# Optimization experiments

Hardware: AMD Instinct MI355X
Metric: run time of the kernel (lower is better)

Reference implementation:

```python
import jax, jax.numpy as jnp
import numpy as np


def setup_inputs() -> dict:
    key = jax.random.key(0)
    k1, k2 = jax.random.split(key)
    B, N, M = 16, 4096, 4096
    points1 = jax.random.normal(k1, (B, N, 3), dtype=jnp.float32)
    points2 = jax.random.normal(k2, (B, M, 3), dtype=jnp.float32)
    return {"points1": points1, "points2": points2}


def reference(points1, points2):
    # Mathematically equal to sum((x - y)^2) without materializing (B,N,M,3).
    w1 = 1.0
    w2 = 1.0
    sq1 = jnp.sum(points1 * points1, axis=-1)  # (B, N)
    sq2 = jnp.sum(points2 * points2, axis=-1)  # (B, M)
    cross = jnp.einsum("bnd,bmd->bnm", points1, points2)  # (B, N, M)
    dist = sq1[:, :, None] + sq2[:, None, :] - 2.0 * cross  # (B, N, M)
    dist_min1 = jnp.min(dist, axis=2)  # nearest in points2 for each point1
    dist_min2 = jnp.min(dist, axis=1)  # nearest in points1 for each point2
    B = points1.shape[0]
    return (w1 * jnp.sum(dist_min1) + w2 * jnp.sum(dist_min2)) / B
```

## Files before the change

### kernel.cpp

```cpp
#include <hip/hip_runtime.h>

typedef _Float16 half8 __attribute__((ext_vector_type(8)));
typedef float f32x16 __attribute__((ext_vector_type(16)));

#define NPTS   4096
#define BATCH  16
#define BLOCK  256
#define CHUNK  2048
#define NCHUNK 2
#define NBLK   512

__global__ __launch_bounds__(BLOCK, 2) void chamfer_mfma_kernel(
    const float* __restrict__ p1, const float* __restrict__ p2,
    float* __restrict__ partial)
{
    __shared__ half8 REC[CHUNK];

    const int tid  = threadIdx.x;
    const int lane = tid & 63;
    const int n    = lane & 31;
    const int grp  = lane >> 5;
    const int wv   = tid >> 6;
    const int blk  = blockIdx.x;
    const int j    = blk & 15;
    const int b    = (blk >> 4) & 15;
    const int dir  = blk >> 8;

    const float* selfp  = (dir == 0 ? p1 : p2) + (size_t)b * NPTS * 3;
    const float* otherp = (dir == 0 ? p2 : p1) + (size_t)b * NPTS * 3;

    const int base = j * 256 + wv * 64;
    half8 a0, a1;
    float ssq01;
    {
        const int i0 = (base + n) * 3, i1 = (base + 32 + n) * 3;
        float x0 = selfp[i0], y0 = selfp[i0 + 1], z0 = selfp[i0 + 2];
        float x1 = selfp[i1], y1 = selfp[i1 + 1], z1 = selfp[i1 + 2];
        ssq01 = fmaf(x0, x0, fmaf(y0, y0, z0 * z0)) +
                fmaf(x1, x1, fmaf(y1, y1, z1 * z1));
        _Float16 hx0 = (_Float16)x0, hy0 = (_Float16)y0, hz0 = (_Float16)z0;
        _Float16 lx0 = (_Float16)(x0 - (float)hx0);
        _Float16 ly0 = (_Float16)(y0 - (float)hy0);
        _Float16 lz0 = (_Float16)(z0 - (float)hz0);
        _Float16 hx1 = (_Float16)x1, hy1 = (_Float16)y1, hz1 = (_Float16)z1;
        _Float16 lx1 = (_Float16)(x1 - (float)hx1);
        _Float16 ly1 = (_Float16)(y1 - (float)hy1);
        _Float16 lz1 = (_Float16)(z1 - (float)hz1);
        const _Float16 c0 = (_Float16)0.f, c1 = (_Float16)1.f;
        if (grp == 0) {
            a0[0]=hx0; a0[1]=hy0; a0[2]=hz0; a0[3]=c0; a0[4]=c0; a0[5]=c0; a0[6]=c1; a0[7]=c0;
            a1[0]=hx1; a1[1]=hy1; a1[2]=hz1; a1[3]=c0; a1[4]=c0; a1[5]=c0; a1[6]=c1; a1[7]=c0;
        } else {
            a0[0]=lx0; a0[1]=ly0; a0[2]=lz0; a0[3]=hx0; a0[4]=hy0; a0[5]=hz0; a0[6]=c0; a0[7]=c1;
            a1[0]=lx1; a1[1]=ly1; a1[2]=lz1; a1[3]=hx1; a1[4]=hy1; a1[5]=hz1; a1[6]=c0; a1[7]=c1;
        }
    }

    f32x16 m0, m1, zc;
#pragma unroll
    for (int r = 0; r < 16; ++r) { m0[r] = 3.4e38f; m1[r] = 3.4e38f; zc[r] = 0.f; }

    for (int c = 0; c < NCHUNK; ++c) {
        __syncthreads();
        {
            const float4* src = (const float4*)(otherp + (size_t)c * CHUNK * 3);
            float4 v0 = src[tid * 6 + 0], v1 = src[tid * 6 + 1];
            float4 v2 = src[tid * 6 + 2], v3 = src[tid * 6 + 3];
            float4 v4 = src[tid * 6 + 4], v5 = src[tid * 6 + 5];
            float ox[8] = {v0.x, v0.w, v1.z, v2.y, v3.x, v3.w, v4.z, v5.y};
            float oy[8] = {v0.y, v1.x, v1.w, v2.z, v3.y, v4.x, v4.w, v5.z};
            float oz[8] = {v0.z, v1.y, v2.x, v2.w, v3.z, v4.y, v5.x, v5.w};
#pragma unroll
            for (int k = 0; k < 8; ++k) {
                float gx = -2.f * ox[k], gy = -2.f * oy[k], gz = -2.f * oz[k];
                float q  = fmaf(ox[k], ox[k], fmaf(oy[k], oy[k], oz[k] * oz[k]));
                _Float16 ghx = (_Float16)gx, ghy = (_Float16)gy, ghz = (_Float16)gz;
                half8 r;
                r[0] = ghx; r[1] = ghy; r[2] = ghz;
                r[3] = (_Float16)(gx - (float)ghx);
                r[4] = (_Float16)(gy - (float)ghy);
                r[5] = (_Float16)(gz - (float)ghz);
                _Float16 qh = (_Float16)q;
                r[6] = qh;
                r[7] = (_Float16)(q - (float)qh);
                REC[tid * 8 + k] = r;
            }
        }
        __syncthreads();
        const half8* rp = REC + n;
#pragma unroll 2
        for (int g = 0; g < 32; ++g) {
            half8 b0 = rp[g * 64];
            half8 b1 = rp[g * 64 + 32];
            f32x16 o00 = __builtin_amdgcn_mfma_f32_32x32x16_f16(a0, b0, zc, 0, 0, 0);
            f32x16 o01 = __builtin_amdgcn_mfma_f32_32x32x16_f16(a0, b1, zc, 0, 0, 0);
            f32x16 o10 = __builtin_amdgcn_mfma_f32_32x32x16_f16(a1, b0, zc, 0, 0, 0);
            f32x16 o11 = __builtin_amdgcn_mfma_f32_32x32x16_f16(a1, b1, zc, 0, 0, 0);
#pragma unroll
            for (int r = 0; r < 16; ++r) {
                m0[r] = fminf(fminf(o00[r], o01[r]), m0[r]);
                m1[r] = fminf(fminf(o10[r], o11[r]), m1[r]);
            }
        }
    }

#pragma unroll
    for (int mask = 1; mask <= 16; mask <<= 1) {
#pragma unroll
        for (int r = 0; r < 16; ++r) {
            m0[r] = fminf(m0[r], __shfl_xor((float)m0[r], mask, 64));
            m1[r] = fminf(m1[r], __shfl_xor((float)m1[r], mask, 64));
        }
    }
    float rowsum = 0.f;
#pragma unroll
    for (int r = 0; r < 16; ++r) rowsum += m0[r] + m1[r];
    rowsum += __shfl_xor(rowsum, 32, 64);

    float sv = grp ? 0.f : ssq01;
#pragma unroll
    for (int mask = 1; mask <= 16; mask <<= 1) sv += __shfl_xor(sv, mask, 64);

    if (lane == 0) partial[blk * 4 + wv] = rowsum + sv;
}

__global__ __launch_bounds__(256) void chamfer_reduce(
    const float* __restrict__ partial, float* __restrict__ out)
{
    float s = 0.f;
    for (int i = threadIdx.x; i < NBLK * 4; i += 256) s += partial[i];
#pragma unroll
    for (int off = 32; off > 0; off >>= 1) s += __shfl_down(s, off, 64);
    __shared__ float ws4[4];
    int lane = threadIdx.x & 63, wv = threadIdx.x >> 6;
    if (lane == 0) ws4[wv] = s;
    __syncthreads();
    if (threadIdx.x == 0)
        out[0] = (ws4[0] + ws4[1] + ws4[2] + ws4[3]) * (1.0f / BATCH);
}

extern "C" void kernel_launch(void* const* d_in, const int* in_sizes, int n_in,
                              void* d_out, int out_size, void* d_ws, size_t ws_size,
                              hipStream_t stream) {
    const float* p1 = (const float*)d_in[0];
    const float* p2 = (const float*)d_in[1];
    float* out = (float*)d_out;
    float* partial = (float*)d_ws;

    chamfer_mfma_kernel<<<dim3(NBLK), dim3(BLOCK), 0, stream>>>(p1, p2, partial);
    chamfer_reduce<<<dim3(1), dim3(256), 0, stream>>>(partial, out);
}
```

Measured before the change: 77.97 us.

## Compute distance tile once for both directions with column atomicMin reductions

Instead of computing the full distance matrix twice (once per direction), each block computes a tile of p1 rows against all p2 points once. It takes row minima in registers and column minima through shuffle plus LDS atomicMin on order-preserving integer keys, then merges them into a global per-batch column-key array. A prep kernel precomputes fp16 hi/lo encodings of p2 into workspace, and the main kernel streams them into LDS with double-buffered global_load_lds. This halves the MFMA work, but adds column reduction ALU, LDS/global atomics, an extra launch and a larger final reduction.

```diff
diff --git a/kernel.cpp b/kernel.cpp
--- a/kernel.cpp
+++ b/kernel.cpp
@@ -1,142 +1,205 @@
 #include <hip/hip_runtime.h>
+#include <stdint.h>
 
 typedef _Float16 half8 __attribute__((ext_vector_type(8)));
 typedef float f32x16 __attribute__((ext_vector_type(16)));
 
 #define NPTS   4096
 #define BATCH  16
-#define BLOCK  256
-#define CHUNK  2048
-#define NCHUNK 2
-#define NBLK   512
-
-__global__ __launch_bounds__(BLOCK, 2) void chamfer_mfma_kernel(
-    const float* __restrict__ p1, const float* __restrict__ p2,
-    float* __restrict__ partial)
+#define TILES  32
+#define BLOCK  512
+#define NBLK   (BATCH * TILES)
+#define CHUNK  1024
+#define NCHUNK (NPTS / CHUNK)
+
+#define REC0_OFF    0
+#define REC1_OFF    (BATCH * NPTS * 16)
+#define COLKEY_OFF  (2 * BATCH * NPTS * 16)
+#define ROWPART_OFF (COLKEY_OFF + BATCH * NPTS * 4)
+
+__device__ __forceinline__ void gll16(const void* g, void* l) {
+    __builtin_amdgcn_global_load_lds(
+        (const __attribute__((address_space(1))) uint32_t*)g,
+        (__attribute__((address_space(3))) uint32_t*)l, 16, 0, 0);
+}
+
+__device__ __forceinline__ uint32_t fkey(float f) {
+    uint32_t u = __float_as_uint(f);
+    return u ^ ((uint32_t)((int32_t)u >> 31) | 0x80000000u);
+}
+__device__ __forceinline__ float funkey(uint32_t k) {
+    uint32_t u = (k & 0x80000000u) ? (k ^ 0x80000000u) : ~k;
+    return __uint_as_float(u);
+}
+
+__device__ __forceinline__ float rmin16(f32x16 o) {
+    float a = fminf(fminf(o[0],  o[1]),  fminf(o[2],  o[3]));
+    float b = fminf(fminf(o[4],  o[5]),  fminf(o[6],  o[7]));
+    float c = fminf(fminf(o[8],  o[9]),  fminf(o[10], o[11]));
+    float d = fminf(fminf(o[12], o[13]), fminf(o[14], o[15]));
+    return fminf(fminf(a, b), fminf(c, d));
+}
+
+__global__ __launch_bounds__(256) void chamfer_prep(
+    const float* __restrict__ p2, uint8_t* __restrict__ ws)
 {
-    __shared__ half8 REC[CHUNK];
+    const int idx = blockIdx.x * 256 + threadIdx.x;
+    const float x = p2[idx * 3], y = p2[idx * 3 + 1], z = p2[idx * 3 + 2];
+    const float gx = -2.f * x, gy = -2.f * y, gz = -2.f * z;
+    const float q  = fmaf(x, x, fmaf(y, y, z * z));
+    _Float16 ghx = (_Float16)gx, ghy = (_Float16)gy, ghz = (_Float16)gz;
+    _Float16 glx = (_Float16)(gx - (float)ghx);
+    _Float16 gly = (_Float16)(gy - (float)ghy);
+    _Float16 glz = (_Float16)(gz - (float)ghz);
+    _Float16 qh = (_Float16)q, ql = (_Float16)(q - (float)qh);
+    const _Float16 one = (_Float16)1.f;
+    half8 r0, r1;
+    r0[0]=ghx; r0[1]=ghy; r0[2]=ghz; r0[3]=one; r0[4]=one; r0[5]=glx; r0[6]=gly; r0[7]=glz;
+    r1[0]=ghx; r1[1]=ghy; r1[2]=ghz; r1[3]=glx; r1[4]=gly; r1[5]=glz; r1[6]=qh;  r1[7]=ql;
+    ((half8*)(ws + REC0_OFF))[idx] = r0;
+    ((half8*)(ws + REC1_OFF))[idx] = r1;
+    ((uint32_t*)(ws + COLKEY_OFF))[idx] = 0xFFFFFFFFu;
+}
+
+__global__ __launch_bounds__(BLOCK, 4) void chamfer_main(
+    const float* __restrict__ p1, uint8_t* __restrict__ ws)
+{
+    __shared__ half8    R0b[2][CHUNK];
+    __shared__ half8    R1b[2][CHUNK];
+    __shared__ uint32_t colKeyL[NPTS];
 
     const int tid  = threadIdx.x;
     const int lane = tid & 63;
     const int n    = lane & 31;
     const int grp  = lane >> 5;
     const int wv   = tid >> 6;
+    const int sg   = wv >> 1;
+    const int gh   = wv & 1;
     const int blk  = blockIdx.x;
-    const int j    = blk & 15;
-    const int b    = (blk >> 4) & 15;
-    const int dir  = blk >> 8;
-
-    const float* selfp  = (dir == 0 ? p1 : p2) + (size_t)b * NPTS * 3;
-    const float* otherp = (dir == 0 ? p2 : p1) + (size_t)b * NPTS * 3;
-
-    const int base = j * 256 + wv * 64;
-    half8 a0, a1;
-    float ssq01;
+    const int tile = blk & (TILES - 1);
+    const int b    = blk >> 5;
+
+    const float* selfp = p1 + (size_t)b * NPTS * 3;
+
+    half8 a;
     {
-        const int i0 = (base + n) * 3, i1 = (base + 32 + n) * 3;
-        float x0 = selfp[i0], y0 = selfp[i0 + 1], z0 = selfp[i0 + 2];
-        float x1 = selfp[i1], y1 = selfp[i1 + 1], z1 = selfp[i1 + 2];
-        ssq01 = fmaf(x0, x0, fmaf(y0, y0, z0 * z0)) +
-                fmaf(x1, x1, fmaf(y1, y1, z1 * z1));
-        _Float16 hx0 = (_Float16)x0, hy0 = (_Float16)y0, hz0 = (_Float16)z0;
-        _Float16 lx0 = (_Float16)(x0 - (float)hx0);
-        _Float16 ly0 = (_Float16)(y0 - (float)hy0);
-        _Float16 lz0 = (_Float16)(z0 - (float)hz0);
-        _Float16 hx1 = (_Float16)x1, hy1 = (_Float16)y1, hz1 = (_Float16)z1;
-        _Float16 lx1 = (_Float16)(x1 - (float)hx1);
-        _Float16 ly1 = (_Float16)(y1 - (float)hy1);
-        _Float16 lz1 = (_Float16)(z1 - (float)hz1);
-        const _Float16 c0 = (_Float16)0.f, c1 = (_Float16)1.f;
-        if (grp == 0) {
-            a0[0]=hx0; a0[1]=hy0; a0[2]=hz0; a0[3]=c0; a0[4]=c0; a0[5]=c0; a0[6]=c1; a0[7]=c0;
-            a1[0]=hx1; a1[1]=hy1; a1[2]=hz1; a1[3]=c0; a1[4]=c0; a1[5]=c0; a1[6]=c1; a1[7]=c0;
-        } else {
-            a0[0]=lx0; a0[1]=ly0; a0[2]=lz0; a0[3]=hx0; a0[4]=hy0; a0[5]=hz0; a0[6]=c0; a0[7]=c1;
-            a1[0]=lx1; a1[1]=ly1; a1[2]=lz1; a1[3]=hx1; a1[4]=hy1; a1[5]=hz1; a1[6]=c0; a1[7]=c1;
+        const int s = tile * 128 + sg * 32 + n;
+        const float x = selfp[s*3], y = selfp[s*3+1], z = selfp[s*3+2];
+        const float ss = fmaf(x, x, fmaf(y, y, z * z));
+        _Float16 hx = (_Float16)x, hy = (_Float16)y, hz = (_Float16)z;
+        _Float16 lx = (_Float16)(x - (float)hx);
+        _Float16 ly = (_Float16)(y - (float)hy);
+        _Float16 lz = (_Float16)(z - (float)hz);
+        _Float16 sh = (_Float16)ss, sl = (_Float16)(ss - (float)sh);
+        const _Float16 one = (_Float16)1.f;
+        if (grp == 0) { a[0]=hx; a[1]=hy; a[2]=hz; a[3]=sh; a[4]=sl; a[5]=lx; a[6]=ly; a[7]=lz; }
+        else          { a[0]=lx; a[1]=ly; a[2]=lz; a[3]=hx; a[4]=hy; a[5]=hz; a[6]=one; a[7]=one; }
+    }
+
+    for (int i = tid; i < NPTS; i += BLOCK) colKeyL[i] = 0xFFFFFFFFu;
+
+    f32x16 m0, zc;
+#pragma unroll
+    for (int r = 0; r < 16; ++r) { m0[r] = 3.4e38f; zc[r] = 0.f; }
+
+    const uint8_t* gsrcBase = ws + (wv < 4 ? REC0_OFF : REC1_OFF)
+                            + (size_t)b * NPTS * 16 + (size_t)(wv & 3) * 4096
+                            + (size_t)lane * 16;
+    {
+        char* l = (char*)(wv < 4 ? &R0b[0][0] : &R1b[0][0]) + (wv & 3) * 4096;
+        const uint8_t* g = gsrcBase;
+        gll16(g, l); gll16(g + 1024, l + 1024);
+        gll16(g + 2048, l + 2048); gll16(g + 3072, l + 3072);
+    }
+    __syncthreads();
+
+    for (int c = 0; c < NCHUNK; ++c) {
+        const int cb = c & 1;
+        if (c + 1 < NCHUNK) {
+            char* l = (char*)(wv < 4 ? &R0b[cb ^ 1][0] : &R1b[cb ^ 1][0]) + (wv & 3) * 4096;
+            const uint8_t* g = gsrcBase + (size_t)(c + 1) * 16384;
+            gll16(g, l); gll16(g + 1024, l + 1024);
+            gll16(g + 2048, l + 2048); gll16(g + 3072, l + 3072);
         }
-    }
-
-    f32x16 m0, m1, zc;
-#pragma unroll
-    for (int r = 0; r < 16; ++r) { m0[r] = 3.4e38f; m1[r] = 3.4e38f; zc[r] = 0.f; }
-
-    for (int c = 0; c < NCHUNK; ++c) {
-        __syncthreads();
-        {
-            const float4* src = (const float4*)(otherp + (size_t)c * CHUNK * 3);
-            float4 v0 = src[tid * 6 + 0], v1 = src[tid * 6 + 1];
-            float4 v2 = src[tid * 6 + 2], v3 = src[tid * 6 + 3];
-            float4 v4 = src[tid * 6 + 4], v5 = src[tid * 6 + 5];
-            float ox[8] = {v0.x, v0.w, v1.z, v2.y, v3.x, v3.w, v4.z, v5.y};
-            float oy[8] = {v0.y, v1.x, v1.w, v2.z, v3.y, v4.x, v4.w, v5.z};
-            float oz[8] = {v0.z, v1.y, v2.x, v2.w, v3.z, v4.y, v5.x, v5.w};
-#pragma unroll
-            for (int k = 0; k < 8; ++k) {
-                float gx = -2.f * ox[k], gy = -2.f * oy[k], gz = -2.f * oz[k];
-                float q  = fmaf(ox[k], ox[k], fmaf(oy[k], oy[k], oz[k] * oz[k]));
-                _Float16 ghx = (_Float16)gx, ghy = (_Float16)gy, ghz = (_Float16)gz;
-                half8 r;
-                r[0] = ghx; r[1] = ghy; r[2] = ghz;
-                r[3] = (_Float16)(gx - (float)ghx);
-                r[4] = (_Float16)(gy - (float)ghy);
-                r[5] = (_Float16)(gz - (float)ghz);
-                _Float16 qh = (_Float16)q;
-                r[6] = qh;
-                r[7] = (_Float16)(q - (float)qh);
-                REC[tid * 8 + k] = r;
-            }
+        const half8* rp = (grp ? &R1b[cb][0] : &R0b[cb][0]) + gh * 512 + n;
+        const int abase = c * CHUNK + gh * 512 + grp * 32 + n;
+#pragma unroll 2
+        for (int k = 0; k < 8; ++k) {
+            half8 b0 = rp[k * 64];
+            half8 b1 = rp[k * 64 + 32];
+            f32x16 o0 = __builtin_amdgcn_mfma_f32_32x32x16_f16(a, b0, zc, 0, 0, 0);
+            f32x16 o1 = __builtin_amdgcn_mfma_f32_32x32x16_f16(a, b1, zc, 0, 0, 0);
+#pragma unroll
+            for (int r = 0; r < 16; ++r)
+                m0[r] = fminf(fminf(o0[r], o1[r]), m0[r]);
+            float c0 = rmin16(o0), c1 = rmin16(o1);
+            c0 = fminf(c0, __shfl_xor(c0, 32));
+            c1 = fminf(c1, __shfl_xor(c1, 32));
+            const float cm = grp ? c1 : c0;
+            atomicMin(&colKeyL[abase + k * 64], fkey(cm));
         }
         __syncthreads();
-        const half8* rp = REC + n;
-#pragma unroll 2
-        for (int g = 0; g < 32; ++g) {
-            half8 b0 = rp[g * 64];
-            half8 b1 = rp[g * 64 + 32];
-            f32x16 o00 = __builtin_amdgcn_mfma_f32_32x32x16_f16(a0, b0, zc, 0, 0, 0);
-            f32x16 o01 = __builtin_amdgcn_mfma_f32_32x32x16_f16(a0, b1, zc, 0, 0, 0);
-            f32x16 o10 = __builtin_amdgcn_mfma_f32_32x32x16_f16(a1, b0, zc, 0, 0, 0);
-            f32x16 o11 = __builtin_amdgcn_mfma_f32_32x32x16_f16(a1, b1, zc, 0, 0, 0);
-#pragma unroll
-            for (int r = 0; r < 16; ++r) {
-                m0[r] = fminf(fminf(o00[r], o01[r]), m0[r]);
-                m1[r] = fminf(fminf(o10[r], o11[r]), m1[r]);
-            }
-        }
-    }
-
-#pragma unroll
-    for (int mask = 1; mask <= 16; mask <<= 1) {
-#pragma unroll
-        for (int r = 0; r < 16; ++r) {
-            m0[r] = fminf(m0[r], __shfl_xor((float)m0[r], mask, 64));
-            m1[r] = fminf(m1[r], __shfl_xor((float)m1[r], mask, 64));
-        }
-    }
-    float rowsum = 0.f;
-#pragma unroll
-    for (int r = 0; r < 16; ++r) rowsum += m0[r] + m1[r];
-    rowsum += __shfl_xor(rowsum, 32, 64);
-
-    float sv = grp ? 0.f : ssq01;
-#pragma unroll
-    for (int mask = 1; mask <= 16; mask <<= 1) sv += __shfl_xor(sv, mask, 64);
-
-    if (lane == 0) partial[blk * 4 + wv] = rowsum + sv;
-}
-
-__global__ __launch_bounds__(256) void chamfer_reduce(
-    const float* __restrict__ partial, float* __restrict__ out)
+    }
+
+#pragma unroll
+    for (int mask = 1; mask <= 16; mask <<= 1)
+#pragma unroll
+        for (int r = 0; r < 16; ++r)
+            m0[r] = fminf(m0[r], __shfl_xor((float)m0[r], mask));
+
+    float* rowminL = (float*)&R0b[0][0];
+    if ((lane & 31) == 0) {
+        const int h = lane >> 5;
+#pragma unroll
+        for (int r = 0; r < 16; ++r)
+            rowminL[wv * 32 + (r & 3) + 8 * (r >> 2) + 4 * h] = m0[r];
+    }
+    uint32_t* colKeyG = (uint32_t*)(ws + COLKEY_OFF) + (size_t)b * NPTS;
+#pragma unroll
+    for (int i = 0; i < NPTS / BLOCK; ++i) {
+        const int m = tid + i * BLOCK;
+        atomicMin(&colKeyG[m], colKeyL[m]);
+    }
+    __syncthreads();
+
+    float* psum = (float*)&R1b[0][0];
+    if (tid < 128) {
+        const int sg2 = tid >> 5, row = tid & 31;
+        float v = fminf(rowminL[(sg2 * 2) * 32 + row],
+                        rowminL[(sg2 * 2 + 1) * 32 + row]);
+#pragma unroll
+        for (int off = 32; off; off >>= 1) v += __shfl_down(v, off);
+        if ((tid & 63) == 0) psum[tid >> 6] = v;
+    }
+    __syncthreads();
+    if (tid == 0)
+        ((float*)(ws + ROWPART_OFF))[blk] = psum[0] + psum[1];
+}
+
+__global__ __launch_bounds__(512) void chamfer_final(
+    const uint8_t* __restrict__ ws, float* __restrict__ out)
 {
+    const uint4* ck = (const uint4*)(ws + COLKEY_OFF);
+    const float* rowpart = (const float*)(ws + ROWPART_OFF);
+    const int tid = threadIdx.x;
     float s = 0.f;
-    for (int i = threadIdx.x; i < NBLK * 4; i += 256) s += partial[i];
-#pragma unroll
-    for (int off = 32; off > 0; off >>= 1) s += __shfl_down(s, off, 64);
-    __shared__ float ws4[4];
-    int lane = threadIdx.x & 63, wv = threadIdx.x >> 6;
-    if (lane == 0) ws4[wv] = s;
-    __syncthreads();
-    if (threadIdx.x == 0)
-        out[0] = (ws4[0] + ws4[1] + ws4[2] + ws4[3]) * (1.0f / BATCH);
+#pragma unroll
+    for (int i = 0; i < 32; ++i) {
+        uint4 v = ck[tid + i * 512];
+        s += funkey(v.x) + funkey(v.y) + funkey(v.z) + funkey(v.w);
+    }
+    s += rowpart[tid];
+#pragma unroll
+    for (int off = 32; off; off >>= 1) s += __shfl_down(s, off);
+    __shared__ float wsum[8];
+    if ((tid & 63) == 0) wsum[tid >> 6] = s;
+    __syncthreads();
+    if (tid == 0) {
+        float t = 0.f;
+#pragma unroll
+        for (int i = 0; i < 8; ++i) t += wsum[i];
+        out[0] = t * (1.0f / BATCH);
+    }
 }
 
 extern "C" void kernel_launch(void* const* d_in, const int* in_sizes, int n_in,
@@ -144,9 +207,8 @@
                               hipStream_t stream) {
     const float* p1 = (const float*)d_in[0];
     const float* p2 = (const float*)d_in[1];
-    float* out = (float*)d_out;
-    float* partial = (float*)d_ws;
-
-    chamfer_mfma_kernel<<<dim3(NBLK), dim3(BLOCK), 0, stream>>>(p1, p2, partial);
-    chamfer_reduce<<<dim3(1), dim3(256), 0, stream>>>(partial, out);
-}
+    uint8_t* ws = (uint8_t*)d_ws;
+    chamfer_prep<<<dim3(256), dim3(256), 0, stream>>>(p2, ws);
+    chamfer_main<<<dim3(NBLK), dim3(BLOCK), 0, stream>>>(p1, ws);
+    chamfer_final<<<dim3(1), dim3(512), 0, stream>>>(ws, (float*)d_out);
+}
```

New measurement: 89.41 us. +14.7%, slower.

## Precompute half8 records in a prep kernel and double-buffer them into LDS

Applied to the files above, without the earlier changes.

Adds a prep kernel that converts all points into split-fp16 distance records in workspace once, rather than having every block recompute them. The main kernel streams those records into double-buffered LDS with async global_load_lds in 1024-point chunks, prefetching the next chunk while MFMAs run on the current one. Each wave now handles 32 self points instead of 64, and the grid doubles to 1024 blocks with a launch bound of 4 blocks per CU, to raise occupancy and spread work. The cost is an extra kernel launch, a workspace round-trip for the records, and less register reuse of each LDS-loaded record per MFMA.

```diff
diff --git a/kernel.cpp b/kernel.cpp
--- a/kernel.cpp
+++ b/kernel.cpp
@@ -1,4 +1,5 @@
 #include <hip/hip_runtime.h>
+#include <stdint.h>
 
 typedef _Float16 half8 __attribute__((ext_vector_type(8)));
 typedef float f32x16 __attribute__((ext_vector_type(16)));
@@ -6,15 +7,48 @@
 #define NPTS   4096
 #define BATCH  16
 #define BLOCK  256
-#define CHUNK  2048
-#define NCHUNK 2
-#define NBLK   512
+#define TILES  32
+#define NBLK   (2 * BATCH * TILES)
+#define CHUNK  1024
+#define NCHUNK (NPTS / CHUNK)
 
-__global__ __launch_bounds__(BLOCK, 2) void chamfer_mfma_kernel(
+#define REC_OFF  0
+#define PART_OFF (2 * BATCH * NPTS * 16)
+
+__device__ __forceinline__ void gll16(const void* g, void* l) {
+    __builtin_amdgcn_global_load_lds(
+        (const __attribute__((address_space(1))) uint32_t*)g,
+        (__attribute__((address_space(3))) uint32_t*)l, 16, 0, 0);
+}
+
+__global__ __launch_bounds__(256) void chamfer_prep(
     const float* __restrict__ p1, const float* __restrict__ p2,
-    float* __restrict__ partial)
+    uint8_t* __restrict__ ws)
 {
-    __shared__ half8 REC[CHUNK];
+    const int idx  = blockIdx.x * 256 + threadIdx.x;
+    const int half = idx >> 16;
+    const int i    = idx & (BATCH * NPTS - 1);
+    const float* src = half ? p1 : p2;
+    const float x = src[i * 3], y = src[i * 3 + 1], z = src[i * 3 + 2];
+    const float gx = -2.f * x, gy = -2.f * y, gz = -2.f * z;
+    const float q  = fmaf(x, x, fmaf(y, y, z * z));
+    _Float16 ghx = (_Float16)gx, ghy = (_Float16)gy, ghz = (_Float16)gz;
+    half8 r;
+    r[0] = ghx; r[1] = ghy; r[2] = ghz;
+    r[3] = (_Float16)(gx - (float)ghx);
+    r[4] = (_Float16)(gy - (float)ghy);
+    r[5] = (_Float16)(gz - (float)ghz);
+    _Float16 qh = (_Float16)q;
+    r[6] = qh;
+    r[7] = (_Float16)(q - (float)qh);
+    ((half8*)(ws + REC_OFF))[idx] = r;
+}
+
+__global__ __launch_bounds__(BLOCK, 4) void chamfer_main(
+    const float* __restrict__ p1, const float* __restrict__ p2,
+    uint8_t* __restrict__ ws)
+{
+    __shared__ half8 RECL[2][CHUNK];
 
     const int tid  = threadIdx.x;
     const int lane = tid & 63;
@@ -22,117 +56,92 @@
     const int grp  = lane >> 5;
     const int wv   = tid >> 6;
     const int blk  = blockIdx.x;
-    const int j    = blk & 15;
-    const int b    = (blk >> 4) & 15;
-    const int dir  = blk >> 8;
+    const int tile = blk & (TILES - 1);
+    const int b    = (blk >> 5) & (BATCH - 1);
+    const int dir  = blk >> 9;
 
-    const float* selfp  = (dir == 0 ? p1 : p2) + (size_t)b * NPTS * 3;
-    const float* otherp = (dir == 0 ? p2 : p1) + (size_t)b * NPTS * 3;
+    const float* selfp = (dir == 0 ? p1 : p2) + (size_t)b * NPTS * 3;
 
-    const int base = j * 256 + wv * 64;
-    half8 a0, a1;
-    float ssq01;
+    half8 a; float ssq;
     {
-        const int i0 = (base + n) * 3, i1 = (base + 32 + n) * 3;
-        float x0 = selfp[i0], y0 = selfp[i0 + 1], z0 = selfp[i0 + 2];
-        float x1 = selfp[i1], y1 = selfp[i1 + 1], z1 = selfp[i1 + 2];
-        ssq01 = fmaf(x0, x0, fmaf(y0, y0, z0 * z0)) +
-                fmaf(x1, x1, fmaf(y1, y1, z1 * z1));
-        _Float16 hx0 = (_Float16)x0, hy0 = (_Float16)y0, hz0 = (_Float16)z0;
-        _Float16 lx0 = (_Float16)(x0 - (float)hx0);
-        _Float16 ly0 = (_Float16)(y0 - (float)hy0);
-        _Float16 lz0 = (_Float16)(z0 - (float)hz0);
-        _Float16 hx1 = (_Float16)x1, hy1 = (_Float16)y1, hz1 = (_Float16)z1;
-        _Float16 lx1 = (_Float16)(x1 - (float)hx1);
-        _Float16 ly1 = (_Float16)(y1 - (float)hy1);
-        _Float16 lz1 = (_Float16)(z1 - (float)hz1);
+        const int s = tile * 128 + wv * 32 + n;
+        const float x = selfp[s * 3], y = selfp[s * 3 + 1], z = selfp[s * 3 + 2];
+        ssq = fmaf(x, x, fmaf(y, y, z * z));
+        _Float16 hx = (_Float16)x, hy = (_Float16)y, hz = (_Float16)z;
+        _Float16 lx = (_Float16)(x - (float)hx);
+        _Float16 ly = (_Float16)(y - (float)hy);
+        _Float16 lz = (_Float16)(z - (float)hz);
         const _Float16 c0 = (_Float16)0.f, c1 = (_Float16)1.f;
-        if (grp == 0) {
-            a0[0]=hx0; a0[1]=hy0; a0[2]=hz0; a0[3]=c0; a0[4]=c0; a0[5]=c0; a0[6]=c1; a0[7]=c0;
-            a1[0]=hx1; a1[1]=hy1; a1[2]=hz1; a1[3]=c0; a1[4]=c0; a1[5]=c0; a1[6]=c1; a1[7]=c0;
-        } else {
-            a0[0]=lx0; a0[1]=ly0; a0[2]=lz0; a0[3]=hx0; a0[4]=hy0; a0[5]=hz0; a0[6]=c0; a0[7]=c1;
-            a1[0]=lx1; a1[1]=ly1; a1[2]=lz1; a1[3]=hx1; a1[4]=hy1; a1[5]=hz1; a1[6]=c0; a1[7]=c1;
-        }
+        if (grp == 0) { a[0]=hx; a[1]=hy; a[2]=hz; a[3]=c0; a[4]=c0; a[5]=c0; a[6]=c1; a[7]=c0; }
+        else          { a[0]=lx; a[1]=ly; a[2]=lz; a[3]=hx; a[4]=hy; a[5]=hz; a[6]=c0; a[7]=c1; }
     }
 
-    f32x16 m0, m1, zc;
+    f32x16 m0, zc;
 #pragma unroll
-    for (int r = 0; r < 16; ++r) { m0[r] = 3.4e38f; m1[r] = 3.4e38f; zc[r] = 0.f; }
+    for (int r = 0; r < 16; ++r) { m0[r] = 3.4e38f; zc[r] = 0.f; }
+
+    const uint8_t* gsrc = ws + REC_OFF
+                        + (((size_t)dir * BATCH + b) * NPTS) * 16
+                        + (size_t)wv * 4096 + (size_t)lane * 16;
+    {
+        char* l = (char*)&RECL[0][0] + wv * 4096;
+        gll16(gsrc, l);            gll16(gsrc + 1024, l + 1024);
+        gll16(gsrc + 2048, l + 2048); gll16(gsrc + 3072, l + 3072);
+    }
+    __syncthreads();
 
     for (int c = 0; c < NCHUNK; ++c) {
-        __syncthreads();
-        {
-            const float4* src = (const float4*)(otherp + (size_t)c * CHUNK * 3);
-            float4 v0 = src[tid * 6 + 0], v1 = src[tid * 6 + 1];
-            float4 v2 = src[tid * 6 + 2], v3 = src[tid * 6 + 3];
-            float4 v4 = src[tid * 6 + 4], v5 = src[tid * 6 + 5];
-            float ox[8] = {v0.x, v0.w, v1.z, v2.y, v3.x, v3.w, v4.z, v5.y};
-            float oy[8] = {v0.y, v1.x, v1.w, v2.z, v3.y, v4.x, v4.w, v5.z};
-            float oz[8] = {v0.z, v1.y, v2.x, v2.w, v3.z, v4.y, v5.x, v5.w};
+        const int cb = c & 1;
+        if (c + 1 < NCHUNK) {
+            char* l = (char*)&RECL[cb ^ 1][0] + wv * 4096;
+            const uint8_t* g = gsrc + (size_t)(c + 1) * (CHUNK * 16);
+            gll16(g, l);            gll16(g + 1024, l + 1024);
+            gll16(g + 2048, l + 2048); gll16(g + 3072, l + 3072);
+        }
+        const half8* rp = &RECL[cb][0] + n;
 #pragma unroll
-            for (int k = 0; k < 8; ++k) {
-                float gx = -2.f * ox[k], gy = -2.f * oy[k], gz = -2.f * oz[k];
-                float q  = fmaf(ox[k], ox[k], fmaf(oy[k], oy[k], oz[k] * oz[k]));
-                _Float16 ghx = (_Float16)gx, ghy = (_Float16)gy, ghz = (_Float16)gz;
-                half8 r;
-                r[0] = ghx; r[1] = ghy; r[2] = ghz;
-                r[3] = (_Float16)(gx - (float)ghx);
-                r[4] = (_Float16)(gy - (float)ghy);
-                r[5] = (_Float16)(gz - (float)ghz);
-                _Float16 qh = (_Float16)q;
-                r[6] = qh;
-                r[7] = (_Float16)(q - (float)qh);
-                REC[tid * 8 + k] = r;
-            }
+        for (int g = 0; g < 32; g += 2) {
+            half8 b0 = rp[g * 32];
+            half8 b1 = rp[g * 32 + 32];
+            f32x16 o0 = __builtin_amdgcn_mfma_f32_32x32x16_f16(a, b0, zc, 0, 0, 0);
+            f32x16 o1 = __builtin_amdgcn_mfma_f32_32x32x16_f16(a, b1, zc, 0, 0, 0);
+#pragma unroll
+            for (int r = 0; r < 16; ++r)
+                m0[r] = fminf(fminf(o0[r], o1[r]), m0[r]);
         }
         __syncthreads();
-        const half8* rp = REC + n;
-#pragma unroll 2
-        for (int g = 0; g < 32; ++g) {
-            half8 b0 = rp[g * 64];
-            half8 b1 = rp[g * 64 + 32];
-            f32x16 o00 = __builtin_amdgcn_mfma_f32_32x32x16_f16(a0, b0, zc, 0, 0, 0);
-            f32x16 o01 = __builtin_amdgcn_mfma_f32_32x32x16_f16(a0, b1, zc, 0, 0, 0);
-            f32x16 o10 = __builtin_amdgcn_mfma_f32_32x32x16_f16(a1, b0, zc, 0, 0, 0);
-            f32x16 o11 = __builtin_amdgcn_mfma_f32_32x32x16_f16(a1, b1, zc, 0, 0, 0);
-#pragma unroll
-            for (int r = 0; r < 16; ++r) {
-                m0[r] = fminf(fminf(o00[r], o01[r]), m0[r]);
-                m1[r] = fminf(fminf(o10[r], o11[r]), m1[r]);
-            }
-        }
     }
 
 #pragma unroll
-    for (int mask = 1; mask <= 16; mask <<= 1) {
+    for (int mask = 1; mask <= 16; mask <<= 1)
 #pragma unroll
-        for (int r = 0; r < 16; ++r) {
-            m0[r] = fminf(m0[r], __shfl_xor((float)m0[r], mask, 64));
-            m1[r] = fminf(m1[r], __shfl_xor((float)m1[r], mask, 64));
-        }
-    }
+        for (int r = 0; r < 16; ++r)
+            m0[r] = fminf(m0[r], __shfl_xor((float)m0[r], mask));
+
     float rowsum = 0.f;
 #pragma unroll
-    for (int r = 0; r < 16; ++r) rowsum += m0[r] + m1[r];
-    rowsum += __shfl_xor(rowsum, 32, 64);
+    for (int r = 0; r < 16; ++r) rowsum += m0[r];
+    rowsum += __shfl_xor(rowsum, 32);
 
-    float sv = grp ? 0.f : ssq01;
+    float sv = grp ? 0.f : ssq;
 #pragma unroll
-    for (int mask = 1; mask <= 16; mask <<= 1) sv += __shfl_xor(sv, mask, 64);
+    for (int mask = 1; mask <= 16; mask <<= 1) sv += __shfl_xor(sv, mask);
 
-    if (lane == 0) partial[blk * 4 + wv] = rowsum + sv;
+    if (lane == 0)
+        ((float*)(ws + PART_OFF))[blk * 4 + wv] = rowsum + sv;
 }
 
 __global__ __launch_bounds__(256) void chamfer_reduce(
-    const float* __restrict__ partial, float* __restrict__ out)
+    const uint8_t* __restrict__ ws, float* __restrict__ out)
 {
+    const float* partial = (const float*)(ws + PART_OFF);
     float s = 0.f;
-    for (int i = threadIdx.x; i < NBLK * 4; i += 256) s += partial[i];
 #pragma unroll
-    for (int off = 32; off > 0; off >>= 1) s += __shfl_down(s, off, 64);
+    for (int i = 0; i < NBLK * 4 / 256; ++i) s += partial[threadIdx.x + i * 256];
+#pragma unroll
+    for (int off = 32; off; off >>= 1) s += __shfl_down(s, off, 64);
     __shared__ float ws4[4];
-    int lane = threadIdx.x & 63, wv = threadIdx.x >> 6;
+    const int lane = threadIdx.x & 63, wv = threadIdx.x >> 6;
     if (lane == 0) ws4[wv] = s;
     __syncthreads();
     if (threadIdx.x == 0)
@@ -144,9 +153,8 @@
                               hipStream_t stream) {
     const float* p1 = (const float*)d_in[0];
     const float* p2 = (const float*)d_in[1];
-    float* out = (float*)d_out;
-    float* partial = (float*)d_ws;
-
-    chamfer_mfma_kernel<<<dim3(NBLK), dim3(BLOCK), 0, stream>>>(p1, p2, partial);
-    chamfer_reduce<<<dim3(1), dim3(256), 0, stream>>>(partial, out);
+    uint8_t* ws = (uint8_t*)d_ws;
+    chamfer_prep<<<dim3(2 * BATCH * NPTS / 256), dim3(256), 0, stream>>>(p1, p2, ws);
+    chamfer_main<<<dim3(NBLK), dim3(BLOCK), 0, stream>>>(p1, p2, ws);
+    chamfer_reduce<<<dim3(1), dim3(256), 0, stream>>>(ws, (float*)d_out);
 }
```

Measured after the change: 78.02 us. Within noise of the previous version (+0.1%).

## Split other-point set across blocks and combine per-row minima in parallel reduce

Applied to the files above, without the earlier changes.

Each block now handles only half of the other point cloud, which doubles the grid to 1024 blocks, drops the chunk loop, and allows occupancy 4 instead of 2. Per-row minima from both halves are written to workspace, and a 128-block reduce kernel takes the min of the two halves, adds the squared norms, and finishes with an atomic-counter last-block sum. The MFMA min updates are interleaved and the LDS layout is changed so stores are conflict-free. The cost is extra global traffic for the per-row partials and a second pass that re-reads the points.

```diff
diff --git a/kernel.cpp b/kernel.cpp
--- a/kernel.cpp
+++ b/kernel.cpp
@@ -1,4 +1,5 @@
 #include <hip/hip_runtime.h>
+#include <stdint.h>
 
 typedef _Float16 half8 __attribute__((ext_vector_type(8)));
 typedef float f32x16 __attribute__((ext_vector_type(16)));
@@ -6,15 +7,20 @@
 #define NPTS   4096
 #define BATCH  16
 #define BLOCK  256
-#define CHUNK  2048
-#define NCHUNK 2
-#define NBLK   512
+#define HOTH   2048
+#define NBLK   1024
+#define RBLK   128
 
-__global__ __launch_bounds__(BLOCK, 2) void chamfer_mfma_kernel(
+#define PART_OFF 0
+#define BSUM_OFF (2 * 2 * BATCH * NPTS * 4)
+#define CNT_OFF  (BSUM_OFF + RBLK * 4)
+
+__global__ __launch_bounds__(BLOCK, 4) void chamfer_main(
     const float* __restrict__ p1, const float* __restrict__ p2,
-    float* __restrict__ partial)
+    uint8_t* __restrict__ ws)
 {
-    __shared__ half8 REC[CHUNK];
+    __shared__ half8 REC[HOTH];
+    __shared__ float ROWS[256];
 
     const int tid  = threadIdx.x;
     const int lane = tid & 63;
@@ -22,22 +28,45 @@
     const int grp  = lane >> 5;
     const int wv   = tid >> 6;
     const int blk  = blockIdx.x;
-    const int j    = blk & 15;
-    const int b    = (blk >> 4) & 15;
-    const int dir  = blk >> 8;
+    const int tile = blk & 15;
+    const int oh   = (blk >> 4) & 1;
+    const int b    = (blk >> 5) & 15;
+    const int dir  = blk >> 9;
 
-    const float* selfp  = (dir == 0 ? p1 : p2) + (size_t)b * NPTS * 3;
-    const float* otherp = (dir == 0 ? p2 : p1) + (size_t)b * NPTS * 3;
+    if (blk == 0 && tid == 0) *(int*)(ws + CNT_OFF) = 0;
 
-    const int base = j * 256 + wv * 64;
+    const float* selfp  = (dir ? p2 : p1) + (size_t)b * NPTS * 3;
+    const float* otherp = (dir ? p1 : p2) + (size_t)b * NPTS * 3 + (size_t)oh * HOTH * 3;
+
+    {
+        const float4* src = (const float4*)otherp;
+        float4 v0 = src[tid*6+0], v1 = src[tid*6+1], v2 = src[tid*6+2];
+        float4 v3 = src[tid*6+3], v4 = src[tid*6+4], v5 = src[tid*6+5];
+        float ox[8] = {v0.x, v0.w, v1.z, v2.y, v3.x, v3.w, v4.z, v5.y};
+        float oy[8] = {v0.y, v1.x, v1.w, v2.z, v3.y, v4.x, v4.w, v5.z};
+        float oz[8] = {v0.z, v1.y, v2.x, v2.w, v3.z, v4.y, v5.x, v5.w};
+#pragma unroll
+        for (int k = 0; k < 8; ++k) {
+            float gx = -2.f * ox[k], gy = -2.f * oy[k], gz = -2.f * oz[k];
+            float q  = fmaf(ox[k], ox[k], fmaf(oy[k], oy[k], oz[k] * oz[k]));
+            _Float16 ghx = (_Float16)gx, ghy = (_Float16)gy, ghz = (_Float16)gz;
+            half8 r;
+            r[0] = ghx; r[1] = ghy; r[2] = ghz;
+            r[3] = (_Float16)(gx - (float)ghx);
+            r[4] = (_Float16)(gy - (float)ghy);
+            r[5] = (_Float16)(gz - (float)ghz);
+            _Float16 qh = (_Float16)q;
+            r[6] = qh;
+            r[7] = (_Float16)(q - (float)qh);
+            REC[k * 256 + tid] = r;
+        }
+    }
+
     half8 a0, a1;
-    float ssq01;
     {
-        const int i0 = (base + n) * 3, i1 = (base + 32 + n) * 3;
+        const int i0 = (tile * 256 + wv * 64 + n) * 3, i1 = i0 + 96;
         float x0 = selfp[i0], y0 = selfp[i0 + 1], z0 = selfp[i0 + 2];
         float x1 = selfp[i1], y1 = selfp[i1 + 1], z1 = selfp[i1 + 2];
-        ssq01 = fmaf(x0, x0, fmaf(y0, y0, z0 * z0)) +
-                fmaf(x1, x1, fmaf(y1, y1, z1 * z1));
         _Float16 hx0 = (_Float16)x0, hy0 = (_Float16)y0, hz0 = (_Float16)z0;
         _Float16 lx0 = (_Float16)(x0 - (float)hx0);
         _Float16 ly0 = (_Float16)(y0 - (float)hy0);
@@ -60,83 +89,85 @@
 #pragma unroll
     for (int r = 0; r < 16; ++r) { m0[r] = 3.4e38f; m1[r] = 3.4e38f; zc[r] = 0.f; }
 
-    for (int c = 0; c < NCHUNK; ++c) {
-        __syncthreads();
-        {
-            const float4* src = (const float4*)(otherp + (size_t)c * CHUNK * 3);
-            float4 v0 = src[tid * 6 + 0], v1 = src[tid * 6 + 1];
-            float4 v2 = src[tid * 6 + 2], v3 = src[tid * 6 + 3];
-            float4 v4 = src[tid * 6 + 4], v5 = src[tid * 6 + 5];
-            float ox[8] = {v0.x, v0.w, v1.z, v2.y, v3.x, v3.w, v4.z, v5.y};
-            float oy[8] = {v0.y, v1.x, v1.w, v2.z, v3.y, v4.x, v4.w, v5.z};
-            float oz[8] = {v0.z, v1.y, v2.x, v2.w, v3.z, v4.y, v5.x, v5.w};
+    __syncthreads();
+
+    const half8* rp = REC + n;
+#pragma unroll 4
+    for (int g = 0; g < 32; ++g) {
+        half8 b0 = rp[g * 64];
+        half8 b1 = rp[g * 64 + 32];
+        f32x16 o00 = __builtin_amdgcn_mfma_f32_32x32x16_f16(a0, b0, zc, 0, 0, 0);
+        f32x16 o01 = __builtin_amdgcn_mfma_f32_32x32x16_f16(a0, b1, zc, 0, 0, 0);
 #pragma unroll
-            for (int k = 0; k < 8; ++k) {
-                float gx = -2.f * ox[k], gy = -2.f * oy[k], gz = -2.f * oz[k];
-                float q  = fmaf(ox[k], ox[k], fmaf(oy[k], oy[k], oz[k] * oz[k]));
-                _Float16 ghx = (_Float16)gx, ghy = (_Float16)gy, ghz = (_Float16)gz;
-                half8 r;
-                r[0] = ghx; r[1] = ghy; r[2] = ghz;
-                r[3] = (_Float16)(gx - (float)ghx);
-                r[4] = (_Float16)(gy - (float)ghy);
-                r[5] = (_Float16)(gz - (float)ghz);
-                _Float16 qh = (_Float16)q;
-                r[6] = qh;
-                r[7] = (_Float16)(q - (float)qh);
-                REC[tid * 8 + k] = r;
-            }
-        }
-        __syncthreads();
-        const half8* rp = REC + n;
-#pragma unroll 2
-        for (int g = 0; g < 32; ++g) {
-            half8 b0 = rp[g * 64];
-            half8 b1 = rp[g * 64 + 32];
-            f32x16 o00 = __builtin_amdgcn_mfma_f32_32x32x16_f16(a0, b0, zc, 0, 0, 0);
-            f32x16 o01 = __builtin_amdgcn_mfma_f32_32x32x16_f16(a0, b1, zc, 0, 0, 0);
-            f32x16 o10 = __builtin_amdgcn_mfma_f32_32x32x16_f16(a1, b0, zc, 0, 0, 0);
-            f32x16 o11 = __builtin_amdgcn_mfma_f32_32x32x16_f16(a1, b1, zc, 0, 0, 0);
+        for (int r = 0; r < 16; ++r)
+            m0[r] = fminf(fminf(o00[r], o01[r]), m0[r]);
+        f32x16 o10 = __builtin_amdgcn_mfma_f32_32x32x16_f16(a1, b0, zc, 0, 0, 0);
+        f32x16 o11 = __builtin_amdgcn_mfma_f32_32x32x16_f16(a1, b1, zc, 0, 0, 0);
 #pragma unroll
-            for (int r = 0; r < 16; ++r) {
-                m0[r] = fminf(fminf(o00[r], o01[r]), m0[r]);
-                m1[r] = fminf(fminf(o10[r], o11[r]), m1[r]);
-            }
-        }
+        for (int r = 0; r < 16; ++r)
+            m1[r] = fminf(fminf(o10[r], o11[r]), m1[r]);
     }
 
 #pragma unroll
-    for (int mask = 1; mask <= 16; mask <<= 1) {
+    for (int mask = 1; mask <= 16; mask <<= 1)
 #pragma unroll
         for (int r = 0; r < 16; ++r) {
-            m0[r] = fminf(m0[r], __shfl_xor((float)m0[r], mask, 64));
-            m1[r] = fminf(m1[r], __shfl_xor((float)m1[r], mask, 64));
+            m0[r] = fminf(m0[r], __shfl_xor((float)m0[r], mask));
+            m1[r] = fminf(m1[r], __shfl_xor((float)m1[r], mask));
+        }
+
+    if (n == 0) {
+#pragma unroll
+        for (int r = 0; r < 16; ++r) {
+            const int row = (r & 3) + 8 * (r >> 2) + 4 * grp;
+            ROWS[wv * 64 + row]      = m0[r];
+            ROWS[wv * 64 + 32 + row] = m1[r];
         }
     }
-    float rowsum = 0.f;
-#pragma unroll
-    for (int r = 0; r < 16; ++r) rowsum += m0[r] + m1[r];
-    rowsum += __shfl_xor(rowsum, 32, 64);
+    __syncthreads();
 
-    float sv = grp ? 0.f : ssq01;
-#pragma unroll
-    for (int mask = 1; mask <= 16; mask <<= 1) sv += __shfl_xor(sv, mask, 64);
-
-    if (lane == 0) partial[blk * 4 + wv] = rowsum + sv;
+    float* part = (float*)(ws + PART_OFF);
+    part[(size_t)oh * (2 * BATCH * NPTS)
+         + ((size_t)dir * BATCH + b) * NPTS + tile * 256 + tid] = ROWS[tid];
 }
 
 __global__ __launch_bounds__(256) void chamfer_reduce(
-    const float* __restrict__ partial, float* __restrict__ out)
+    const float* __restrict__ p1, const float* __restrict__ p2,
+    uint8_t* __restrict__ ws, float* __restrict__ out)
 {
+    const float* part = (const float*)(ws + PART_OFF);
+    float* bsum = (float*)(ws + BSUM_OFF);
+    int*   cnt  = (int*)(ws + CNT_OFF);
+
+    const int t0 = blockIdx.x * 256 + threadIdx.x;
     float s = 0.f;
-    for (int i = threadIdx.x; i < NBLK * 4; i += 256) s += partial[i];
 #pragma unroll
-    for (int off = 32; off > 0; off >>= 1) s += __shfl_down(s, off, 64);
+    for (int i = 0; i < 4; ++i) {
+        const int gs  = t0 + i * 32768;
+        const int dir = gs >> 16;
+        const int rem = gs & 65535;
+        const float* pp = (dir ? p2 : p1) + (size_t)rem * 3;
+        const float x = pp[0], y = pp[1], z = pp[2];
+        const float ssq = fmaf(x, x, fmaf(y, y, z * z));
+        s += fminf(part[gs], part[2 * BATCH * NPTS + gs]) + ssq;
+    }
+#pragma unroll
+    for (int off = 32; off; off >>= 1) s += __shfl_down(s, off, 64);
     __shared__ float ws4[4];
-    int lane = threadIdx.x & 63, wv = threadIdx.x >> 6;
-    if (lane == 0) ws4[wv] = s;
+    if ((threadIdx.x & 63) == 0) ws4[threadIdx.x >> 6] = s;
     __syncthreads();
-    if (threadIdx.x == 0)
-        out[0] = (ws4[0] + ws4[1] + ws4[2] + ws4[3]) * (1.0f / BATCH);
+    if (threadIdx.x == 0) {
+        bsum[blockIdx.x] = ws4[0] + ws4[1] + ws4[2] + ws4[3];
+        __threadfence();
+        const int old = atomicAdd(cnt, 1);
+        if (old == RBLK - 1) {
+            __threadfence();
+            const volatile float* vb = (const volatile float*)bsum;
+            float tot = 0.f;
+            for (int i = 0; i < RBLK; ++i) tot += vb[i];
+            out[0] = tot * (1.0f / BATCH);
+        }
+    }
 }
 
 extern "C" void kernel_launch(void* const* d_in, const int* in_sizes, int n_in,
@@ -144,9 +175,7 @@
                               hipStream_t stream) {
     const float* p1 = (const float*)d_in[0];
     const float* p2 = (const float*)d_in[1];
-    float* out = (float*)d_out;
-    float* partial = (float*)d_ws;
-
-    chamfer_mfma_kernel<<<dim3(NBLK), dim3(BLOCK), 0, stream>>>(p1, p2, partial);
-    chamfer_reduce<<<dim3(1), dim3(256), 0, stream>>>(partial, out);
+    uint8_t* ws = (uint8_t*)d_ws;
+    chamfer_main<<<dim3(NBLK), dim3(BLOCK), 0, stream>>>(p1, p2, ws);
+    chamfer_reduce<<<dim3(RBLK), dim3(256), 0, stream>>>(p1, p2, ws, (float*)d_out);
 }
```

After: 111.7 us. 1.43x slower.
